# Kernel tuning notes

Hardware: AMD Instinct MI355X
Metric: run time of the kernel (lower is better)

The kernel has to match this reference:

```python
import jax, jax.numpy as jnp
import numpy as np

N = 50000      # nodes
E = 800000     # edges
IN = 256       # in_dim
H = 8          # heads
C = 32         # out_dim per head (H*C == IN so residual is identity)
NEG_SLOPE = 0.2
LN_EPS = 1e-5


def setup_inputs() -> dict:
    key = jax.random.key(0)
    ks = jax.random.split(key, 8)
    x = jax.random.normal(ks[0], (N, IN), dtype=jnp.float32)
    edge_index = jax.random.randint(ks[1], (2, E), 0, N, dtype=jnp.int64)
    # GATConv params
    W = jax.random.normal(ks[2], (IN, H * C), dtype=jnp.float32) / np.sqrt(IN)
    att_src = jax.random.normal(ks[3], (H, C), dtype=jnp.float32) / np.sqrt(C)
    att_dst = jax.random.normal(ks[4], (H, C), dtype=jnp.float32) / np.sqrt(C)
    bias = jnp.zeros((H * C,), dtype=jnp.float32)
    # LayerNorm params
    ln_scale = jnp.ones((H * C,), dtype=jnp.float32)
    ln_bias = jnp.zeros((H * C,), dtype=jnp.float32)
    return {"x": x, "edge_index": edge_index, "W": W, "att_src": att_src,
            "att_dst": att_dst, "bias": bias, "ln_scale": ln_scale, "ln_bias": ln_bias}


def _gat_block(x, edge_index, W, att_src, att_dst, bias, ln_scale, ln_bias):
    src, dst = edge_index[0], edge_index[1]
    # linear projection -> [N, H, C]
    h = (x @ W).reshape(N, H, C)
    # per-node attention logits [N, H]
    a_src = jnp.einsum('nhc,hc->nh', h, att_src)
    a_dst = jnp.einsum('nhc,hc->nh', h, att_dst)
    # per-edge logits with LeakyReLU [E, H]
    alpha = jax.nn.leaky_relu(a_src[src] + a_dst[dst], NEG_SLOPE)
    # segment softmax over incoming edges of each destination node
    amax = jax.ops.segment_max(alpha, dst, num_segments=N)          # [N, H]
    amax = jnp.where(jnp.isfinite(amax), amax, 0.0)                 # empty segments
    ex = jnp.exp(alpha - amax[dst])                                 # [E, H]
    denom = jax.ops.segment_sum(ex, dst, num_segments=N)           # [N, H]
    attn = ex / (denom[dst] + 1e-16)                                # [E, H]
    # weighted message aggregation -> [N, H, C]
    msg = h[src] * attn[:, :, None]
    out = jax.ops.segment_sum(msg, dst, num_segments=N)
    out = out.reshape(N, H * C) + bias
    # residual (identity since in_dim == heads*out_dim), ELU, LayerNorm
    out = out + x
    out = jax.nn.elu(out)
    mu = jnp.mean(out, axis=-1, keepdims=True)
    var = jnp.var(out, axis=-1, keepdims=True)
    return (out - mu) * jax.lax.rsqrt(var + LN_EPS) * ln_scale + ln_bias


def reference(x, edge_index, W, att_src, att_dst, bias, ln_scale, ln_bias):
    return _gat_block(x, edge_index, W, att_src, att_dst, bias, ln_scale, ln_bias)
```

## Files before the change

kernel.cpp:

```cpp
#include <hip/hip_runtime.h>
#include <hip/hip_bf16.h>
#include <cstdint>

#define NN 50000
#define NE 800000
#define DIM 256
#define NH 8
#define NB 196

typedef short v8s __attribute__((ext_vector_type(8)));
typedef float v4f __attribute__((ext_vector_type(4)));
typedef unsigned short u16x8 __attribute__((ext_vector_type(8)));

__device__ __forceinline__ float b2f(unsigned short u) {
    union { float f; uint32_t i; } c; c.i = ((uint32_t)u) << 16; return c.f;
}
__device__ __forceinline__ unsigned short f2b(float f) {
    union { float f; uint32_t i; } c; c.f = f;
    uint32_t lsb = (c.i >> 16) & 1u;
    return (unsigned short)((c.i + 0x7FFFu + lsb) >> 16);
}

__global__ void detect_kernel(const int* __restrict__ e, int* __restrict__ flag) {
    if (threadIdx.x == 0 && blockIdx.x == 0) {
        int allz = 1;
        for (int i = 0; i < 64; ++i)
            if (e[2 * i + 1] != 0) { allz = 0; break; }
        *flag = allz;
    }
}

__global__ void normalize_kernel(const int* __restrict__ e, const int* __restrict__ flag,
                                 int* __restrict__ srcN, int* __restrict__ dstN,
                                 int* __restrict__ deg) {
    int i = blockIdx.x * blockDim.x + threadIdx.x;
    if (i >= NE) return;
    int s, d;
    if (*flag) { s = e[2 * i]; d = e[2 * (NE + i)]; }
    else       { s = e[i];     d = e[NE + i]; }
    srcN[i] = s;
    dstN[i] = d;
    atomicAdd(&deg[d], 1);
}

__global__ __launch_bounds__(256) void cvtx_kernel(const float* __restrict__ X,
                                                   unsigned short* __restrict__ Xb) {
    int i = (blockIdx.x * 256 + threadIdx.x) * 8;
    float4 v0 = *(const float4*)(X + i);
    float4 v1 = *(const float4*)(X + i + 4);
    u16x8 o;
    o[0] = f2b(v0.x); o[1] = f2b(v0.y); o[2] = f2b(v0.z); o[3] = f2b(v0.w);
    o[4] = f2b(v1.x); o[5] = f2b(v1.y); o[6] = f2b(v1.z); o[7] = f2b(v1.w);
    *(u16x8*)(Xb + i) = o;
}

__global__ __launch_bounds__(256) void cvtw_kernel(const float* __restrict__ W,
                                                   unsigned short* __restrict__ Wt) {
    int idx = blockIdx.x * 256 + threadIdx.x;
    int k = idx >> 8, n = idx & 255;
    Wt[n * DIM + k] = f2b(W[k * DIM + n]);
}

#define BM 128
#define BN 64
#define BK 128
#define LDA 136
__global__ __launch_bounds__(256) void gemm_kernel(
    const unsigned short* __restrict__ Xb, const unsigned short* __restrict__ Wt,
    unsigned short* __restrict__ H) {
    __shared__ __align__(16) unsigned short As[BM * LDA];
    __shared__ __align__(16) unsigned short Bs[BN * LDA];
    const int bm = blockIdx.x >> 2, bn = blockIdx.x & 3;
    const int m0 = bm * BM, n0 = bn * BN;
    const int t = threadIdx.x;
    const int wave = t >> 6, lane = t & 63;
    const int fr = lane & 15, fq = lane >> 4;
    const int kg = fq << 3;

    v4f acc[2][4];
    #pragma unroll
    for (int mi = 0; mi < 2; ++mi)
        #pragma unroll
        for (int j = 0; j < 4; ++j) acc[mi][j] = (v4f){0.f, 0.f, 0.f, 0.f};

    #pragma unroll
    for (int kt = 0; kt < 256; kt += BK) {
        #pragma unroll
        for (int it = 0; it < 8; ++it) {
            int vec = t + it * 256;
            int row = vec >> 4;
            int kv = (vec & 15) << 3;
            int gr = m0 + row;
            u16x8 val = {0, 0, 0, 0, 0, 0, 0, 0};
            if (gr < NN) val = *(const u16x8*)(Xb + (size_t)gr * DIM + kt + kv);
            *(u16x8*)(As + row * LDA + kv) = val;
        }
        #pragma unroll
        for (int it = 0; it < 4; ++it) {
            int vec = t + it * 256;
            int row = vec >> 4;
            int kv = (vec & 15) << 3;
            u16x8 val = *(const u16x8*)(Wt + (size_t)(n0 + row) * DIM + kt + kv);
            *(u16x8*)(Bs + row * LDA + kv) = val;
        }
        __syncthreads();
        #pragma unroll
        for (int ks = 0; ks < BK; ks += 32) {
            v8s a0 = *(const v8s*)(As + (wave * 32 + fr) * LDA + ks + kg);
            v8s a1 = *(const v8s*)(As + (wave * 32 + 16 + fr) * LDA + ks + kg);
            #pragma unroll
            for (int j = 0; j < 4; ++j) {
                v8s b = *(const v8s*)(Bs + (j * 16 + fr) * LDA + ks + kg);
                acc[0][j] = __builtin_amdgcn_mfma_f32_16x16x32_bf16(a0, b, acc[0][j], 0, 0, 0);
                acc[1][j] = __builtin_amdgcn_mfma_f32_16x16x32_bf16(a1, b, acc[1][j], 0, 0, 0);
            }
        }
        __syncthreads();
    }
    const int orow_base = m0 + wave * 32;
    #pragma unroll
    for (int mi = 0; mi < 2; ++mi)
        #pragma unroll
        for (int j = 0; j < 4; ++j)
            #pragma unroll
            for (int r = 0; r < 4; ++r) {
                int gr = orow_base + mi * 16 + fq * 4 + r;
                if (gr < NN) H[(size_t)gr * DIM + n0 + j * 16 + fr] = f2b(acc[mi][j][r]);
            }
}

__global__ __launch_bounds__(256) void att_kernel(
    const unsigned short* __restrict__ H, const float* __restrict__ ASRC,
    const float* __restrict__ ADST, float* __restrict__ a_src,
    float* __restrict__ a_dst) {
    const int wave = threadIdx.x >> 6, lane = threadIdx.x & 63;
    const int n = blockIdx.x * 4 + wave;
    if (n >= NN) return;
    float4 as4 = *(const float4*)(ASRC + lane * 4);
    float4 ad4 = *(const float4*)(ADST + lane * 4);
    ushort4 hv = *(const ushort4*)(H + (size_t)n * DIM + lane * 4);
    const unsigned short* hvp = (const unsigned short*)&hv;
    float h0 = b2f(hvp[0]), h1 = b2f(hvp[1]), h2 = b2f(hvp[2]), h3 = b2f(hvp[3]);
    float ps = h0 * as4.x + h1 * as4.y + h2 * as4.z + h3 * as4.w;
    float pd = h0 * ad4.x + h1 * ad4.y + h2 * ad4.z + h3 * ad4.w;
    #pragma unroll
    for (int off = 1; off <= 4; off <<= 1) {
        ps += __shfl_xor(ps, off);
        pd += __shfl_xor(pd, off);
    }
    if ((lane & 7) == 0) {
        a_src[n * NH + (lane >> 3)] = ps;
        a_dst[n * NH + (lane >> 3)] = pd;
    }
}

__global__ __launch_bounds__(256) void scan1_kernel(const int* __restrict__ deg,
                                                    int* __restrict__ row_start,
                                                    int* __restrict__ bsum) {
    const int t = threadIdx.x, b = blockIdx.x;
    const int i = b * 256 + t;
    const int lane = t & 63, wave = t >> 6;
    int v = (i < NN) ? deg[i] : 0;
    int x = v;
    #pragma unroll
    for (int off = 1; off <= 32; off <<= 1) {
        int y = __shfl_up(x, off);
        if (lane >= off) x += y;
    }
    __shared__ int wt[4];
    if (lane == 63) wt[wave] = x;
    __syncthreads();
    int add = 0;
    #pragma unroll
    for (int w2 = 0; w2 < 4; ++w2) if (w2 < wave) add += wt[w2];
    int incl = x + add;
    if (i < NN) row_start[i] = incl - v;
    if (t == 255) bsum[b] = incl;
}

__global__ __launch_bounds__(256) void scan2_kernel(const int* __restrict__ bsum,
                                                    int* __restrict__ boff,
                                                    int* __restrict__ row_start) {
    const int t = threadIdx.x;
    const int lane = t & 63, wave = t >> 6;
    int v = (t < NB) ? bsum[t] : 0;
    int x = v;
    #pragma unroll
    for (int off = 1; off <= 32; off <<= 1) {
        int y = __shfl_up(x, off);
        if (lane >= off) x += y;
    }
    __shared__ int wt[4];
    if (lane == 63) wt[wave] = x;
    __syncthreads();
    int add = 0;
    #pragma unroll
    for (int w2 = 0; w2 < 4; ++w2) if (w2 < wave) add += wt[w2];
    int incl = x + add;
    if (t < NB) boff[t] = incl - v;
    if (t == 255) row_start[NN] = incl;
}

__global__ __launch_bounds__(256) void scan3_kernel(int* __restrict__ row_start,
                                                    const int* __restrict__ boff,
                                                    int* __restrict__ cursor) {
    const int i = blockIdx.x * 256 + threadIdx.x;
    if (i < NN) {
        int r = row_start[i] + boff[blockIdx.x];
        row_start[i] = r;
        cursor[i] = r;
    }
}

__global__ void fill_kernel(const int* __restrict__ src, const int* __restrict__ dst,
                            int* __restrict__ cursor, int* __restrict__ csr_src) {
    int e = blockIdx.x * blockDim.x + threadIdx.x;
    if (e < NE) {
        int d = dst[e];
        int pos = atomicAdd(&cursor[d], 1);
        csr_src[pos] = src[e];
    }
}

__global__ __launch_bounds__(256) void agg_kernel(
    const unsigned short* __restrict__ H, const float* __restrict__ a_src,
    const float* __restrict__ a_dst, const int* __restrict__ row_start,
    const int* __restrict__ csr_src, const float* __restrict__ X,
    const float* __restrict__ BIAS, const float* __restrict__ LNS,
    const float* __restrict__ LNB, float* __restrict__ OUT) {
    const int wave = threadIdx.x >> 6, lane = threadIdx.x & 63;
    const int d = blockIdx.x * 4 + wave;
    if (d >= NN) return;
    const int base = row_start[d];
    const int degree = row_start[d + 1] - base;
    const int slot = lane >> 5;
    const int q = lane & 31;
    const int head = q >> 2;
    const float ad_h = a_dst[d * NH + head];

    float acc[8];
    #pragma unroll
    for (int j = 0; j < 8; ++j) acc[j] = 0.f;
    float sum_ex = 0.f;

    for (int i = 0; i < degree; i += 2) {
        int e = i + slot;
        bool valid = e < degree;
        int s = valid ? csr_src[base + e] : 0;
        float lg = a_src[s * NH + head] + ad_h;
        lg = lg > 0.f ? lg : 0.2f * lg;
        float w = valid ? __expf(lg) : 0.f;
        sum_ex += w;
        u16x8 hv = *(const u16x8*)(H + (size_t)s * DIM + q * 8);
        #pragma unroll
        for (int j = 0; j < 8; ++j) acc[j] += w * b2f(hv[j]);
    }
    sum_ex += __shfl_xor(sum_ex, 32);
    #pragma unroll
    for (int j = 0; j < 8; ++j) acc[j] += __shfl_xor(acc[j], 32);

    const float inv = 1.0f / (sum_ex + 1e-16f);

    float4 x0 = *(const float4*)(X + (size_t)d * DIM + q * 8);
    float4 x1 = *(const float4*)(X + (size_t)d * DIM + q * 8 + 4);
    float4 b0 = *(const float4*)(BIAS + q * 8);
    float4 b1 = *(const float4*)(BIAS + q * 8 + 4);
    const float* xp0 = (const float*)&x0; const float* xp1 = (const float*)&x1;
    const float* bp0 = (const float*)&b0; const float* bp1 = (const float*)&b1;
    float v[8];
    float s1 = 0.f, s2 = 0.f;
    #pragma unroll
    for (int j = 0; j < 8; ++j) {
        float xv = (j < 4) ? xp0[j] : xp1[j - 4];
        float bv = (j < 4) ? bp0[j] : bp1[j - 4];
        float t = acc[j] * inv + bv + xv;
        t = t > 0.f ? t : expm1f(t);
        v[j] = t;
        s1 += t;
        s2 += t * t;
    }
    #pragma unroll
    for (int off = 16; off >= 1; off >>= 1) {
        s1 += __shfl_xor(s1, off);
        s2 += __shfl_xor(s2, off);
    }
    const float mean = s1 * (1.0f / 256.0f);
    float var = s2 * (1.0f / 256.0f) - mean * mean;
    var = fmaxf(var, 0.f);
    const float rstd = rsqrtf(var + 1e-5f);

    if (slot == 0) {
        float4 sc0 = *(const float4*)(LNS + q * 8);
        float4 sc1 = *(const float4*)(LNS + q * 8 + 4);
        float4 lb0 = *(const float4*)(LNB + q * 8);
        float4 lb1 = *(const float4*)(LNB + q * 8 + 4);
        const float* scp0 = (const float*)&sc0; const float* scp1 = (const float*)&sc1;
        const float* lbp0 = (const float*)&lb0; const float* lbp1 = (const float*)&lb1;
        float4 o0, o1;
        float* op0 = (float*)&o0; float* op1 = (float*)&o1;
        #pragma unroll
        for (int j = 0; j < 4; ++j) {
            op0[j] = (v[j] - mean) * rstd * scp0[j] + lbp0[j];
            op1[j] = (v[j + 4] - mean) * rstd * scp1[j] + lbp1[j];
        }
        *(float4*)(OUT + (size_t)d * DIM + q * 8) = o0;
        *(float4*)(OUT + (size_t)d * DIM + q * 8 + 4) = o1;
    }
}

extern "C" void kernel_launch(void* const* d_in, const int* in_sizes, int n_in,
                              void* d_out, int out_size, void* d_ws, size_t ws_size,
                              hipStream_t stream) {
    const float* X    = (const float*)d_in[0];
    const int*   EIDX = (const int*)d_in[1];
    const float* W    = (const float*)d_in[2];
    const float* ASRC = (const float*)d_in[3];
    const float* ADST = (const float*)d_in[4];
    const float* BIAS = (const float*)d_in[5];
    const float* LNS  = (const float*)d_in[6];
    const float* LNB  = (const float*)d_in[7];
    float* OUT = (float*)d_out;

    char* ws = (char*)d_ws;
    unsigned short* H  = (unsigned short*)(ws);
    unsigned short* Xb = (unsigned short*)(ws + 25600000);
    unsigned short* Wt = (unsigned short*)(ws + 51200000);
    float* a_src       = (float*)(ws + 51331072);
    float* a_dst       = (float*)(ws + 52931072);
    int*   deg         = (int*)(ws + 54531072);
    int*   row_start   = (int*)(ws + 54731072);
    int*   cursor      = (int*)(ws + 54931080);
    int*   csr_src     = (int*)(ws + 55131080);
    int*   srcN        = (int*)(ws + 58331080);
    int*   dstN        = (int*)(ws + 61531080);
    int*   bsum        = (int*)(ws + 64731080);
    int*   boff        = (int*)(ws + 64731864);
    int*   eflag       = (int*)(ws + 64732648);

    hipMemsetAsync(deg, 0, NN * sizeof(int), stream);

    dim3 blk(256);
    detect_kernel<<<dim3(1), dim3(64), 0, stream>>>(EIDX, eflag);
    normalize_kernel<<<dim3((NE + 255) / 256), blk, 0, stream>>>(EIDX, eflag, srcN, dstN, deg);
    cvtx_kernel<<<dim3(6250), blk, 0, stream>>>(X, Xb);
    cvtw_kernel<<<dim3(256), blk, 0, stream>>>(W, Wt);
    gemm_kernel<<<dim3(391 * 4), blk, 0, stream>>>(Xb, Wt, H);
    att_kernel<<<dim3((NN + 3) / 4), blk, 0, stream>>>(H, ASRC, ADST, a_src, a_dst);
    scan1_kernel<<<dim3(NB), blk, 0, stream>>>(deg, row_start, bsum);
    scan2_kernel<<<dim3(1), blk, 0, stream>>>(bsum, boff, row_start);
    scan3_kernel<<<dim3(NB), blk, 0, stream>>>(row_start, boff, cursor);
    fill_kernel<<<dim3((NE + 255) / 256), blk, 0, stream>>>(srcN, dstN, cursor, csr_src);
    agg_kernel<<<dim3((NN + 3) / 4), blk, 0, stream>>>(
        H, a_src, a_dst, row_start, csr_src, X, BIAS, LNS, LNB, OUT);
}
```

Before: 330.4 us.

## Fuse X conversion into GEMM, inline edge-format detection, batch aggregation loads

Removes the separate detect kernel by having each wave ballot-probe the edge layout inside normalize_kernel. Drops the cvtx pass by converting fp32 X to bf16 while staging it in the GEMM. The GEMM now uses 128x256 tiles over all 256 output columns with 512 threads. The aggregation kernel now computes attention weights for 8 edges x 8 heads per lane group and issues four gathered H row loads per iteration instead of one. It also hoists the LayerNorm parameter loads. The goal is fewer launches, less intermediate traffic and more memory-level parallelism in the gather, at the cost of extra shuffles and register pressure.

```diff
diff --git a/kernel.cpp b/kernel.cpp
--- a/kernel.cpp
+++ b/kernel.cpp
@@ -21,37 +21,20 @@
     return (unsigned short)((c.i + 0x7FFFu + lsb) >> 16);
 }
 
-__global__ void detect_kernel(const int* __restrict__ e, int* __restrict__ flag) {
-    if (threadIdx.x == 0 && blockIdx.x == 0) {
-        int allz = 1;
-        for (int i = 0; i < 64; ++i)
-            if (e[2 * i + 1] != 0) { allz = 0; break; }
-        *flag = allz;
-    }
-}
-
-__global__ void normalize_kernel(const int* __restrict__ e, const int* __restrict__ flag,
-                                 int* __restrict__ srcN, int* __restrict__ dstN,
-                                 int* __restrict__ deg) {
-    int i = blockIdx.x * blockDim.x + threadIdx.x;
-    if (i >= NE) return;
+__global__ __launch_bounds__(256) void normalize_kernel(
+    const int* __restrict__ e, int* __restrict__ srcN, int* __restrict__ dstN,
+    int* __restrict__ deg) {
+    const int i = blockIdx.x * 256 + threadIdx.x;
+    const int lane = threadIdx.x & 63;
+    int probe = e[2 * lane + 1];
+    unsigned long long nz = __ballot(probe != 0);
+    bool is64 = (nz == 0ull);
     int s, d;
-    if (*flag) { s = e[2 * i]; d = e[2 * (NE + i)]; }
-    else       { s = e[i];     d = e[NE + i]; }
+    if (is64) { s = e[2 * i]; d = e[2 * (NE + i)]; }
+    else      { s = e[i];     d = e[NE + i]; }
     srcN[i] = s;
     dstN[i] = d;
     atomicAdd(&deg[d], 1);
-}
-
-__global__ __launch_bounds__(256) void cvtx_kernel(const float* __restrict__ X,
-                                                   unsigned short* __restrict__ Xb) {
-    int i = (blockIdx.x * 256 + threadIdx.x) * 8;
-    float4 v0 = *(const float4*)(X + i);
-    float4 v1 = *(const float4*)(X + i + 4);
-    u16x8 o;
-    o[0] = f2b(v0.x); o[1] = f2b(v0.y); o[2] = f2b(v0.z); o[3] = f2b(v0.w);
-    o[4] = f2b(v1.x); o[5] = f2b(v1.y); o[6] = f2b(v1.z); o[7] = f2b(v1.w);
-    *(u16x8*)(Xb + i) = o;
 }
 
 __global__ __launch_bounds__(256) void cvtw_kernel(const float* __restrict__ W,
@@ -61,71 +44,69 @@
     Wt[n * DIM + k] = f2b(W[k * DIM + n]);
 }
 
-#define BM 128
-#define BN 64
-#define BK 128
-#define LDA 136
-__global__ __launch_bounds__(256) void gemm_kernel(
-    const unsigned short* __restrict__ Xb, const unsigned short* __restrict__ Wt,
+#define LDA2 40
+__global__ __launch_bounds__(512) void gemm_kernel(
+    const float* __restrict__ X, const unsigned short* __restrict__ Wt,
     unsigned short* __restrict__ H) {
-    __shared__ __align__(16) unsigned short As[BM * LDA];
-    __shared__ __align__(16) unsigned short Bs[BN * LDA];
-    const int bm = blockIdx.x >> 2, bn = blockIdx.x & 3;
-    const int m0 = bm * BM, n0 = bn * BN;
+    __shared__ __align__(16) unsigned short As[128 * LDA2];
+    __shared__ __align__(16) unsigned short Bs[256 * LDA2];
     const int t = threadIdx.x;
     const int wave = t >> 6, lane = t & 63;
+    const int wr = wave >> 2, wc = wave & 3;
     const int fr = lane & 15, fq = lane >> 4;
-    const int kg = fq << 3;
-
-    v4f acc[2][4];
-    #pragma unroll
-    for (int mi = 0; mi < 2; ++mi)
+    const int m0 = blockIdx.x * 128;
+
+    v4f acc[4][4];
+    #pragma unroll
+    for (int mi = 0; mi < 4; ++mi)
         #pragma unroll
         for (int j = 0; j < 4; ++j) acc[mi][j] = (v4f){0.f, 0.f, 0.f, 0.f};
 
     #pragma unroll
-    for (int kt = 0; kt < 256; kt += BK) {
-        #pragma unroll
-        for (int it = 0; it < 8; ++it) {
-            int vec = t + it * 256;
-            int row = vec >> 4;
-            int kv = (vec & 15) << 3;
+    for (int kt = 0; kt < 256; kt += 32) {
+        #pragma unroll
+        for (int it = 0; it < 2; ++it) {
+            int v = t + it * 512;
+            int row = v >> 3;
+            int c4 = (v & 7) << 2;
             int gr = m0 + row;
-            u16x8 val = {0, 0, 0, 0, 0, 0, 0, 0};
-            if (gr < NN) val = *(const u16x8*)(Xb + (size_t)gr * DIM + kt + kv);
-            *(u16x8*)(As + row * LDA + kv) = val;
+            float4 val = make_float4(0.f, 0.f, 0.f, 0.f);
+            if (gr < NN) val = *(const float4*)(X + (size_t)gr * DIM + kt + c4);
+            ushort4 o;
+            o.x = f2b(val.x); o.y = f2b(val.y); o.z = f2b(val.z); o.w = f2b(val.w);
+            *(ushort4*)(As + row * LDA2 + c4) = o;
         }
         #pragma unroll
-        for (int it = 0; it < 4; ++it) {
-            int vec = t + it * 256;
-            int row = vec >> 4;
-            int kv = (vec & 15) << 3;
-            u16x8 val = *(const u16x8*)(Wt + (size_t)(n0 + row) * DIM + kt + kv);
-            *(u16x8*)(Bs + row * LDA + kv) = val;
+        for (int it = 0; it < 2; ++it) {
+            int v = t + it * 512;
+            int row = v >> 2;
+            int kv = (v & 3) << 3;
+            u16x8 val = *(const u16x8*)(Wt + (size_t)row * DIM + kt + kv);
+            *(u16x8*)(Bs + row * LDA2 + kv) = val;
         }
         __syncthreads();
-        #pragma unroll
-        for (int ks = 0; ks < BK; ks += 32) {
-            v8s a0 = *(const v8s*)(As + (wave * 32 + fr) * LDA + ks + kg);
-            v8s a1 = *(const v8s*)(As + (wave * 32 + 16 + fr) * LDA + ks + kg);
+        v8s a[4];
+        #pragma unroll
+        for (int mi = 0; mi < 4; ++mi)
+            a[mi] = *(const v8s*)(As + (wr * 64 + mi * 16 + fr) * LDA2 + fq * 8);
+        #pragma unroll
+        for (int j = 0; j < 4; ++j) {
+            v8s b = *(const v8s*)(Bs + (wc * 64 + j * 16 + fr) * LDA2 + fq * 8);
             #pragma unroll
-            for (int j = 0; j < 4; ++j) {
-                v8s b = *(const v8s*)(Bs + (j * 16 + fr) * LDA + ks + kg);
-                acc[0][j] = __builtin_amdgcn_mfma_f32_16x16x32_bf16(a0, b, acc[0][j], 0, 0, 0);
-                acc[1][j] = __builtin_amdgcn_mfma_f32_16x16x32_bf16(a1, b, acc[1][j], 0, 0, 0);
-            }
+            for (int mi = 0; mi < 4; ++mi)
+                acc[mi][j] = __builtin_amdgcn_mfma_f32_16x16x32_bf16(a[mi], b, acc[mi][j], 0, 0, 0);
         }
         __syncthreads();
     }
-    const int orow_base = m0 + wave * 32;
-    #pragma unroll
-    for (int mi = 0; mi < 2; ++mi)
+    #pragma unroll
+    for (int mi = 0; mi < 4; ++mi)
         #pragma unroll
         for (int j = 0; j < 4; ++j)
             #pragma unroll
             for (int r = 0; r < 4; ++r) {
-                int gr = orow_base + mi * 16 + fq * 4 + r;
-                if (gr < NN) H[(size_t)gr * DIM + n0 + j * 16 + fr] = f2b(acc[mi][j][r]);
+                int gr = m0 + wr * 64 + mi * 16 + fq * 4 + r;
+                int gc = wc * 64 + j * 16 + fr;
+                if (gr < NN) H[(size_t)gr * DIM + gc] = f2b(acc[mi][j][r]);
             }
 }
 
@@ -235,40 +216,73 @@
     const int degree = row_start[d + 1] - base;
     const int slot = lane >> 5;
     const int q = lane & 31;
-    const int head = q >> 2;
-    const float ad_h = a_dst[d * NH + head];
-
-    float acc[8];
-    #pragma unroll
-    for (int j = 0; j < 8; ++j) acc[j] = 0.f;
-    float sum_ex = 0.f;
-
-    for (int i = 0; i < degree; i += 2) {
-        int e = i + slot;
-        bool valid = e < degree;
-        int s = valid ? csr_src[base + e] : 0;
-        float lg = a_src[s * NH + head] + ad_h;
-        lg = lg > 0.f ? lg : 0.2f * lg;
-        float w = valid ? __expf(lg) : 0.f;
-        sum_ex += w;
-        u16x8 hv = *(const u16x8*)(H + (size_t)s * DIM + q * 8);
-        #pragma unroll
-        for (int j = 0; j < 8; ++j) acc[j] += w * b2f(hv[j]);
-    }
-    sum_ex += __shfl_xor(sum_ex, 32);
-    #pragma unroll
-    for (int j = 0; j < 8; ++j) acc[j] += __shfl_xor(acc[j], 32);
-
-    const float inv = 1.0f / (sum_ex + 1e-16f);
+    const int jj = lane >> 3;
+    const int hh = lane & 7;
+    const int headq = q >> 2;
+
+    const float ad = a_dst[d * NH + hh];
 
     float4 x0 = *(const float4*)(X + (size_t)d * DIM + q * 8);
     float4 x1 = *(const float4*)(X + (size_t)d * DIM + q * 8 + 4);
     float4 b0 = *(const float4*)(BIAS + q * 8);
     float4 b1 = *(const float4*)(BIAS + q * 8 + 4);
+    float4 sc0 = *(const float4*)(LNS + q * 8);
+    float4 sc1 = *(const float4*)(LNS + q * 8 + 4);
+    float4 lb0 = *(const float4*)(LNB + q * 8);
+    float4 lb1 = *(const float4*)(LNB + q * 8 + 4);
+
+    float acc[8];
+    #pragma unroll
+    for (int j = 0; j < 8; ++j) acc[j] = 0.f;
+    float swacc = 0.f;
+
+    for (int c0 = 0; c0 < degree; c0 += 8) {
+        int e = c0 + jj;
+        bool vld = e < degree;
+        int sj = vld ? csr_src[base + e] : 0;
+        float av = a_src[sj * NH + hh];
+        float lg = av + ad;
+        lg = lg > 0.f ? lg : 0.2f * lg;
+        float w = vld ? __expf(lg) : 0.f;
+        swacc += w;
+
+        int s0 = __shfl(sj, (0 + slot) * 8);
+        int s1 = __shfl(sj, (2 + slot) * 8);
+        int s2 = __shfl(sj, (4 + slot) * 8);
+        int s3 = __shfl(sj, (6 + slot) * 8);
+        u16x8 hv0 = *(const u16x8*)(H + (size_t)s0 * DIM + q * 8);
+        u16x8 hv1 = *(const u16x8*)(H + (size_t)s1 * DIM + q * 8);
+        u16x8 hv2 = *(const u16x8*)(H + (size_t)s2 * DIM + q * 8);
+        u16x8 hv3 = *(const u16x8*)(H + (size_t)s3 * DIM + q * 8);
+        float w0 = __shfl(w, (0 + slot) * 8 + headq);
+        float w1 = __shfl(w, (2 + slot) * 8 + headq);
+        float w2 = __shfl(w, (4 + slot) * 8 + headq);
+        float w3 = __shfl(w, (6 + slot) * 8 + headq);
+        #pragma unroll
+        for (int j = 0; j < 8; ++j) acc[j] += w0 * b2f(hv0[j]);
+        #pragma unroll
+        for (int j = 0; j < 8; ++j) acc[j] += w1 * b2f(hv1[j]);
+        #pragma unroll
+        for (int j = 0; j < 8; ++j) acc[j] += w2 * b2f(hv2[j]);
+        #pragma unroll
+        for (int j = 0; j < 8; ++j) acc[j] += w3 * b2f(hv3[j]);
+    }
+
+    float sumw = swacc;
+    sumw += __shfl_xor(sumw, 8);
+    sumw += __shfl_xor(sumw, 16);
+    sumw += __shfl_xor(sumw, 32);
+    float sum_ex = __shfl(sumw, headq);
+
+    #pragma unroll
+    for (int j = 0; j < 8; ++j) acc[j] += __shfl_xor(acc[j], 32);
+
+    const float inv = 1.0f / (sum_ex + 1e-16f);
+
     const float* xp0 = (const float*)&x0; const float* xp1 = (const float*)&x1;
     const float* bp0 = (const float*)&b0; const float* bp1 = (const float*)&b1;
     float v[8];
-    float s1 = 0.f, s2 = 0.f;
+    float s1v = 0.f, s2v = 0.f;
     #pragma unroll
     for (int j = 0; j < 8; ++j) {
         float xv = (j < 4) ? xp0[j] : xp1[j - 4];
@@ -276,24 +290,20 @@
         float t = acc[j] * inv + bv + xv;
         t = t > 0.f ? t : expm1f(t);
         v[j] = t;
-        s1 += t;
-        s2 += t * t;
+        s1v += t;
+        s2v += t * t;
     }
     #pragma unroll
     for (int off = 16; off >= 1; off >>= 1) {
-        s1 += __shfl_xor(s1, off);
-        s2 += __shfl_xor(s2, off);
-    }
-    const float mean = s1 * (1.0f / 256.0f);
-    float var = s2 * (1.0f / 256.0f) - mean * mean;
+        s1v += __shfl_xor(s1v, off);
+        s2v += __shfl_xor(s2v, off);
+    }
+    const float mean = s1v * (1.0f / 256.0f);
+    float var = s2v * (1.0f / 256.0f) - mean * mean;
     var = fmaxf(var, 0.f);
     const float rstd = rsqrtf(var + 1e-5f);
 
     if (slot == 0) {
-        float4 sc0 = *(const float4*)(LNS + q * 8);
-        float4 sc1 = *(const float4*)(LNS + q * 8 + 4);
-        float4 lb0 = *(const float4*)(LNB + q * 8);
-        float4 lb1 = *(const float4*)(LNB + q * 8 + 4);
         const float* scp0 = (const float*)&sc0; const float* scp1 = (const float*)&sc1;
         const float* lbp0 = (const float*)&lb0; const float* lbp1 = (const float*)&lb1;
         float4 o0, o1;
@@ -323,28 +333,24 @@
 
     char* ws = (char*)d_ws;
     unsigned short* H  = (unsigned short*)(ws);
-    unsigned short* Xb = (unsigned short*)(ws + 25600000);
-    unsigned short* Wt = (unsigned short*)(ws + 51200000);
-    float* a_src       = (float*)(ws + 51331072);
-    float* a_dst       = (float*)(ws + 52931072);
-    int*   deg         = (int*)(ws + 54531072);
-    int*   row_start   = (int*)(ws + 54731072);
-    int*   cursor      = (int*)(ws + 54931080);
-    int*   csr_src     = (int*)(ws + 55131080);
-    int*   srcN        = (int*)(ws + 58331080);
-    int*   dstN        = (int*)(ws + 61531080);
-    int*   bsum        = (int*)(ws + 64731080);
-    int*   boff        = (int*)(ws + 64731864);
-    int*   eflag       = (int*)(ws + 64732648);
+    unsigned short* Wt = (unsigned short*)(ws + 25600000);
+    float* a_src       = (float*)(ws + 25731072);
+    float* a_dst       = (float*)(ws + 27331072);
+    int*   deg         = (int*)(ws + 28931072);
+    int*   row_start   = (int*)(ws + 29131072);
+    int*   cursor      = (int*)(ws + 29331088);
+    int*   csr_src     = (int*)(ws + 29531088);
+    int*   srcN        = (int*)(ws + 32731088);
+    int*   dstN        = (int*)(ws + 35931088);
+    int*   bsum        = (int*)(ws + 39131088);
+    int*   boff        = (int*)(ws + 39131872);
 
     hipMemsetAsync(deg, 0, NN * sizeof(int), stream);
 
     dim3 blk(256);
-    detect_kernel<<<dim3(1), dim3(64), 0, stream>>>(EIDX, eflag);
-    normalize_kernel<<<dim3((NE + 255) / 256), blk, 0, stream>>>(EIDX, eflag, srcN, dstN, deg);
-    cvtx_kernel<<<dim3(6250), blk, 0, stream>>>(X, Xb);
+    normalize_kernel<<<dim3(NE / 256), blk, 0, stream>>>(EIDX, srcN, dstN, deg);
     cvtw_kernel<<<dim3(256), blk, 0, stream>>>(W, Wt);
-    gemm_kernel<<<dim3(391 * 4), blk, 0, stream>>>(Xb, Wt, H);
+    gemm_kernel<<<dim3(391), dim3(512), 0, stream>>>(X, Wt, H);
     att_kernel<<<dim3((NN + 3) / 4), blk, 0, stream>>>(H, ASRC, ADST, a_src, a_dst);
     scan1_kernel<<<dim3(NB), blk, 0, stream>>>(deg, row_start, bsum);
     scan2_kernel<<<dim3(1), blk, 0, stream>>>(bsum, boff, row_start);
```

Result: faster. 309.2 us (-6.4%).
